# Kernel tuning notes

Hardware: AMD Instinct MI355X
Metric: run time of the kernel (lower is better)

Reference implementation:

```python
import jax, jax.numpy as jnp
import numpy as np

N_ATOM, N_CHI, N_BOND, N_DIR = 119, 3, 5, 3
NUM_LAYER, EMB, FEAT, NG = 5, 300, 256, 4096
N_NODES, N_EDGES = 100000, 200000


def setup_inputs() -> dict:
    key = jax.random.key(0)
    ks = jax.random.split(key, 16)
    N, E = N_NODES, N_EDGES
    r = lambda k, s, sc: jax.random.normal(k, s, jnp.float32) * sc
    inp = {}
    inp["atom_type"] = jax.random.randint(ks[0], (N,), 0, N_ATOM, dtype=jnp.int32)
    inp["chirality"] = jax.random.randint(ks[1], (N,), 0, N_CHI, dtype=jnp.int32)
    inp["edge_index"] = jax.random.randint(ks[2], (2, E), 0, N, dtype=jnp.int32)
    inp["edge_type"] = jax.random.randint(ks[3], (E,), 0, 4, dtype=jnp.int32)
    inp["edge_dir"] = jax.random.randint(ks[4], (E,), 0, N_DIR, dtype=jnp.int32)
    inp["batch"] = jnp.sort(jax.random.randint(ks[5], (N,), 0, NG, dtype=jnp.int32))
    inp["atom_emb1"] = r(ks[6], (N_ATOM, EMB), 0.02)
    inp["atom_emb2"] = r(ks[7], (N_CHI, EMB), 0.02)
    inp["W"] = r(ks[8], (NUM_LAYER, EMB, EMB), 0.05)
    inp["b"] = jnp.zeros((NUM_LAYER, EMB), jnp.float32)
    inp["ee1"] = r(ks[9], (NUM_LAYER, N_BOND, 1), 0.5)
    inp["ee2"] = r(ks[10], (NUM_LAYER, N_DIR, 1), 0.5)
    inp["bn_gamma"] = jnp.ones((NUM_LAYER, EMB), jnp.float32)
    inp["bn_beta"] = jnp.zeros((NUM_LAYER, EMB), jnp.float32)
    inp["feat_W"] = r(ks[11], (EMB, FEAT), 0.05)
    inp["feat_b"] = jnp.zeros((FEAT,), jnp.float32)
    inp["head_W1"] = r(ks[12], (FEAT, FEAT // 2), 0.08)
    inp["head_b1"] = jnp.zeros((FEAT // 2,), jnp.float32)
    inp["head_W2"] = r(ks[13], (FEAT // 2, 2), 0.1)
    inp["head_b2"] = jnp.zeros((2,), jnp.float32)
    return inp


def reference(atom_type, chirality, edge_index, edge_type, edge_dir, batch,
              atom_emb1, atom_emb2, W, b, ee1, ee2, bn_gamma, bn_beta,
              feat_W, feat_b, head_W1, head_b1, head_W2, head_b2):
    N = atom_type.shape[0]
    # add self loops (edge_attr: bond_type=4, direction=0)
    loops = jnp.arange(N, dtype=edge_index.dtype)
    row = jnp.concatenate([edge_index[0], loops])
    col = jnp.concatenate([edge_index[1], loops])
    et = jnp.concatenate([edge_type, jnp.full((N,), 4, edge_type.dtype)])
    ed = jnp.concatenate([edge_dir, jnp.zeros((N,), edge_dir.dtype)])

    h = atom_emb1[atom_type] + atom_emb2[chirality]  # [N, EMB]
    for l in range(NUM_LAYER):
        hx = h @ W[l]                                  # [N, EMB]
        edge_emb = ee1[l][et] + ee2[l][ed]             # [E+N, 1]
        msg = hx[row] + edge_emb                       # gather + broadcast add
        out = jax.ops.segment_sum(msg, col, num_segments=N) + b[l]
        # BatchNorm1d (training-mode batch stats, eps=1e-5)
        mean = out.mean(axis=0)
        var = out.var(axis=0)
        h = bn_gamma[l] * (out - mean) * jax.lax.rsqrt(var + 1e-5) + bn_beta[l]
        if l < NUM_LAYER - 1:
            h = jax.nn.relu(h)  # drop_ratio=0 -> dropout is identity

    # global mean pool over graphs
    sums = jax.ops.segment_sum(h, batch, num_segments=NG)              # [NG, EMB]
    counts = jax.ops.segment_sum(jnp.ones((N, 1), h.dtype), batch, num_segments=NG)
    hg = sums / jnp.maximum(counts, 1.0)

    hf = hg @ feat_W + feat_b                                          # [NG, FEAT]
    pred = jax.nn.softplus(hf @ head_W1 + head_b1) @ head_W2 + head_b2  # [NG, 2]
    return hf, pred
```

## Files before the change

kernel.cpp:

```cpp
#include <hip/hip_runtime.h>
#include <math.h>

typedef unsigned short u16;
typedef unsigned int u32;
typedef short v8s __attribute__((ext_vector_type(8)));
typedef float v4f __attribute__((ext_vector_type(4)));

#define EMB 300
#define SP 320
#define NGRP 4096
#define FEAT 256
#define MT 128
#define NT 160
#define NCOMB 357
#define NREP 32
#define CSB (NREP * 2 * SP)

__device__ __forceinline__ u16 f2bf(float x) {
    u32 u = __float_as_uint(x);
    u += 0x7FFFu + ((u >> 16) & 1u);
    return (u16)(u >> 16);
}
__device__ __forceinline__ float bf2f(u16 h) {
    return __uint_as_float((u32)h << 16);
}
__device__ __forceinline__ void unpack8(uint4 w, float* o) {
    const u32* p = &w.x;
#pragma unroll
    for (int q = 0; q < 4; q++) {
        o[2 * q]     = __uint_as_float(p[q] << 16);
        o[2 * q + 1] = __uint_as_float(p[q] & 0xFFFF0000u);
    }
}
__device__ __forceinline__ v8s clampA(uint4 w, float4 ta, float4 tb) {
    const u32* p = &w.x;
    float t[8] = {ta.x, ta.y, ta.z, ta.w, tb.x, tb.y, tb.z, tb.w};
    u32 o[4];
#pragma unroll
    for (int q = 0; q < 4; q++) {
        float lo = __uint_as_float(p[q] << 16);
        float hi = __uint_as_float(p[q] & 0xFFFF0000u);
        lo = fmaxf(lo, t[2 * q]);
        hi = fmaxf(hi, t[2 * q + 1]);
        o[q] = (__float_as_uint(lo) >> 16) | (__float_as_uint(hi) & 0xFFFF0000u);
    }
    uint4 r = make_uint4(o[0], o[1], o[2], o[3]);
    return *(v8s*)&r;
}
__device__ __forceinline__ void dma16(const u16* g, u16* l) {
    __builtin_amdgcn_global_load_lds(
        (const __attribute__((address_space(1))) unsigned int*)g,
        (__attribute__((address_space(3))) unsigned int*)l, 16, 0, 0);
}

__global__ void k_prep_n(const int* __restrict__ at, const int* __restrict__ ch,
                         int* __restrict__ c9, int* __restrict__ deg,
                         int* __restrict__ cursor, float* __restrict__ cs0, int N) {
    int n = blockIdx.x * blockDim.x + threadIdx.x;
    if (n < N) {
        c9[n] = at[n] * 3 + ch[n];
        deg[n] = 0;
        cursor[n] = 0;
    }
    if (n < CSB) cs0[n] = 0.f;
}

__global__ void k_count(const int* __restrict__ col, int* __restrict__ deg, int E) {
    int e = blockIdx.x * blockDim.x + threadIdx.x;
    if (e < E) atomicAdd(&deg[col[e]], 1);
}

__global__ __launch_bounds__(256) void k_bsum(const int* __restrict__ deg,
                                              int* __restrict__ bsum, int N) {
    int base = blockIdx.x * 1024 + threadIdx.x * 4;
    int s = 0;
    if (base + 3 < N) {
        int4 v = *(const int4*)(deg + base);
        s = v.x + v.y + v.z + v.w;
    } else {
        for (int j = 0; j < 4; j++) if (base + j < N) s += deg[base + j];
    }
    __shared__ int red[256];
    red[threadIdx.x] = s;
    __syncthreads();
    for (int off = 128; off > 0; off >>= 1) {
        if (threadIdx.x < off) red[threadIdx.x] += red[threadIdx.x + off];
        __syncthreads();
    }
    if (threadIdx.x == 0) bsum[blockIdx.x] = red[0];
}

__global__ __launch_bounds__(128) void k_scanb(const int* __restrict__ bsum,
                                               int* __restrict__ boff, int NB) {
    __shared__ int sh[128];
    int t = threadIdx.x;
    int v = (t < NB) ? bsum[t] : 0;
    sh[t] = v;
    __syncthreads();
    for (int off = 1; off < 128; off <<= 1) {
        int add = (t >= off) ? sh[t - off] : 0;
        __syncthreads();
        sh[t] += add;
        __syncthreads();
    }
    if (t < NB) boff[t] = sh[t] - v;
}

__global__ __launch_bounds__(256) void k_indptr(const int* __restrict__ deg,
                                                const int* __restrict__ boff,
                                                int* __restrict__ indptr, int N) {
    int b = blockIdx.x, t = threadIdx.x;
    int base = b * 1024 + t * 4;
    int v[4] = {0, 0, 0, 0};
    if (base + 3 < N) {
        int4 w = *(const int4*)(deg + base);
        v[0] = w.x; v[1] = w.y; v[2] = w.z; v[3] = w.w;
    } else {
        for (int j = 0; j < 4; j++) if (base + j < N) v[j] = deg[base + j];
    }
    int tsum = v[0] + v[1] + v[2] + v[3];
    __shared__ int sh[256];
    sh[t] = tsum;
    __syncthreads();
    for (int off = 1; off < 256; off <<= 1) {
        int add = (t >= off) ? sh[t - off] : 0;
        __syncthreads();
        sh[t] += add;
        __syncthreads();
    }
    int run = boff[b] + sh[t] - tsum;
    for (int j = 0; j < 4; j++) {
        run += v[j];
        if (base + j < N) indptr[base + j + 1] = run;
    }
    if (b == 0 && t == 0) indptr[0] = 0;
}

__global__ void k_fill(const int* __restrict__ row, const int* __restrict__ col,
                       const int* __restrict__ et, const int* __restrict__ ed,
                       const int* __restrict__ indptr, int* __restrict__ cursor,
                       int* __restrict__ packed, int E) {
    int e = blockIdx.x * blockDim.x + threadIdx.x;
    if (e >= E) return;
    int c = col[e];
    int pos = indptr[c] + atomicAdd(&cursor[c], 1);
    packed[pos] = row[e] | ((et[e] * 3 + ed[e]) << 17);
}

__global__ void k_comb(const float* __restrict__ e1, const float* __restrict__ e2,
                       u16* __restrict__ comb) {
    int idx = blockIdx.x * blockDim.x + threadIdx.x;
    if (idx >= NCOMB * 40) return;
    int row = idx / 40, f = idx % 40;
    int at = row / 3, ch = row % 3;
    u32 o[4];
#pragma unroll
    for (int q = 0; q < 4; q++) {
        int c0 = f * 8 + q * 2;
        float x0 = 0.f, x1 = 0.f;
        if (c0 < EMB)     x0 = e1[(size_t)at * EMB + c0] + e2[(size_t)ch * EMB + c0];
        if (c0 + 1 < EMB) x1 = e1[(size_t)at * EMB + c0 + 1] + e2[(size_t)ch * EMB + c0 + 1];
        o[q] = (u32)f2bf(x0) | ((u32)f2bf(x1) << 16);
    }
    *(uint4*)(comb + (size_t)row * SP + f * 8) = make_uint4(o[0], o[1], o[2], o[3]);
}

__global__ __launch_bounds__(320) void k_wprep(
    const float* __restrict__ Wl, const float* __restrict__ cs,
    const float* __restrict__ gamma, const float* __restrict__ beta,
    int ident, int N, u16* __restrict__ Wt, float* __restrict__ srow,
    float* __restrict__ thr) {
    __shared__ float wred[5];
    int n = blockIdx.x;
    int k = threadIdx.x;
    float scv, shv, thv;
    if (ident) {
        scv = (k < EMB) ? 1.f : 0.f;
        shv = 0.f;
        thv = -__builtin_inff();
    } else if (k < EMB) {
        float s1 = 0.f, s2 = 0.f;
        for (int r = 0; r < NREP; r++) {
            s1 += cs[r * 2 * SP + k];
            s2 += cs[r * 2 * SP + SP + k];
        }
        float inv = 1.f / (float)N;
        float mean = s1 * inv;
        float var = s2 * inv - mean * mean;
        float rstd = rsqrtf(fmaxf(var, 0.f) + 1e-5f);
        scv = gamma[k] * rstd;
        shv = beta[k] - mean * scv;
        thv = bf2f(f2bf(-shv / scv));
    } else {
        scv = 0.f; shv = 0.f; thv = -__builtin_inff();
    }
    if (n == 0) thr[k] = thv;

    float w = 0.f;
    if (n < EMB && k < EMB) w = Wl[(size_t)k * EMB + n];
    Wt[(size_t)n * SP + k] = f2bf(w * scv);
    float s = (k < EMB) ? shv * w : 0.f;
#pragma unroll
    for (int o2 = 32; o2 > 0; o2 >>= 1) s += __shfl_down(s, o2);
    if ((k & 63) == 0) wred[k >> 6] = s;
    __syncthreads();
    if (k == 0) {
        float t = wred[0] + wred[1] + wred[2] + wred[3] + wred[4];
        srow[n] = (n < EMB) ? t : 0.f;
    }
}

__global__ void k_finalize(const float* __restrict__ cs,
                           const float* __restrict__ gamma, const float* __restrict__ beta,
                           float* __restrict__ sc, float* __restrict__ sh, int N) {
    int c = threadIdx.x;
    if (c >= SP) return;
    float s1 = 0.f, s2 = 0.f;
    for (int r = 0; r < NREP; r++) {
        s1 += cs[r * 2 * SP + c];
        s2 += cs[r * 2 * SP + SP + c];
    }
    if (c < EMB) {
        float inv = 1.f / (float)N;
        float mean = s1 * inv;
        float var = s2 * inv - mean * mean;
        float rstd = rsqrtf(fmaxf(var, 0.f) + 1e-5f);
        float s = gamma[c] * rstd;
        sc[c] = s;
        sh[c] = beta[c] - mean * s;
    } else {
        sc[c] = 0.f; sh[c] = 0.f;
    }
}

__global__ __launch_bounds__(256) void k_gemm(
    const u16* __restrict__ A, const u16* __restrict__ Wt,
    const float* __restrict__ thr, const float* __restrict__ srow,
    u16* __restrict__ C, int M, const int* __restrict__ rowmap,
    float* __restrict__ zbank) {
    __shared__ __align__(16) u16 sm[18432];

    int m0 = blockIdx.y * MT;
    int n0 = blockIdx.x * NT;
    int tid = threadIdx.x;
    int wave = tid >> 6, lane = tid & 63;
    int wm = wave >> 1, wn = wave & 1;
    int lm = lane & 15, quad = lane >> 4;

    if (blockIdx.x == 0 && blockIdx.y == 0)
        for (int i = tid; i < CSB; i += 256) zbank[i] = 0.f;

    int ar0 = min(m0 + (tid >> 2), M - 1);
    int ar1 = min(m0 + 64 + (tid >> 2), M - 1);
    if (rowmap) { ar0 = rowmap[ar0]; ar1 = rowmap[ar1]; }
    const u16* ag0 = A + (size_t)ar0 * SP + (tid & 3) * 8;
    const u16* ag1 = A + (size_t)ar1 * SP + (tid & 3) * 8;
    const u16* bg0 = Wt + (size_t)(n0 + (tid >> 2)) * SP + (tid & 3) * 8;
    const u16* bg1 = Wt + (size_t)(n0 + 64 + (tid >> 2)) * SP + (tid & 3) * 8;
    const u16* bg2 = Wt + (size_t)(n0 + 128 + (tid >> 2)) * SP + (tid & 3) * 8;

    const float* tp = thr + quad * 8;

    v4f acc[4][5];
#pragma unroll
    for (int nf = 0; nf < 5; nf++) {
        float sv = srow[n0 + wn * 80 + nf * 16 + lm];
#pragma unroll
        for (int mf = 0; mf < 4; mf++)
            acc[mf][nf] = (v4f){sv, sv, sv, sv};
    }

    auto issue = [&](int d, int kt) {
        int ko = kt * 32;
        u16* ad = sm + d * 4096;
        u16* bd = sm + 8192 + d * 5120;
        dma16(ag0 + ko, ad + tid * 8);
        dma16(ag1 + ko, ad + (256 + tid) * 8);
        dma16(bg0 + ko, bd + tid * 8);
        dma16(bg1 + ko, bd + (256 + tid) * 8);
        if (tid < 128) dma16(bg2 + ko, bd + (512 + tid) * 8);
    };

    issue(0, 0);
    for (int kt = 0; kt < SP / 32; kt++) {
        __syncthreads();
        if (kt + 1 < SP / 32) issue((kt + 1) & 1, kt + 1);
        const u16* as = sm + (kt & 1) * 4096;
        const u16* bs = sm + 8192 + (kt & 1) * 5120;
        float4 ta = *(const float4*)(tp + kt * 32);
        float4 tb = *(const float4*)(tp + kt * 32 + 4);
        v8s b[5], a[4];
#pragma unroll
        for (int nf = 0; nf < 5; nf++)
            b[nf] = *(const v8s*)(bs + (wn * 80 + nf * 16 + lm) * 32 + quad * 8);
#pragma unroll
        for (int mf = 0; mf < 4; mf++) {
            uint4 w = *(const uint4*)(as + (wm * 64 + mf * 16 + lm) * 32 + quad * 8);
            a[mf] = clampA(w, ta, tb);
        }
#pragma unroll
        for (int nf = 0; nf < 5; nf++)
#pragma unroll
            for (int mf = 0; mf < 4; mf++)
                acc[mf][nf] = __builtin_amdgcn_mfma_f32_16x16x32_bf16(a[mf], b[nf], acc[mf][nf], 0, 0, 0);
    }

    __syncthreads();
#pragma unroll
    for (int p = 0; p < 2; p++) {
#pragma unroll
        for (int mf2 = 0; mf2 < 2; mf2++) {
            int mf = p * 2 + mf2;
#pragma unroll
            for (int nf = 0; nf < 5; nf++)
#pragma unroll
                for (int r = 0; r < 4; r++)
                    sm[(wm * 32 + mf2 * 16 + quad * 4 + r) * 168 + wn * 80 + nf * 16 + lm] =
                        f2bf(acc[mf][nf][r]);
        }
        __syncthreads();
#pragma unroll
        for (int i = 0; i < 5; i++) {
            int slot = tid + i * 256;
            int lr = slot / 20, cg = slot % 20;
            int grow = m0 + (lr >> 5) * 64 + p * 32 + (lr & 31);
            if (grow < M)
                *(uint4*)(C + (size_t)grow * SP + n0 + cg * 8) =
                    *(const uint4*)(sm + lr * 168 + cg * 8);
        }
        __syncthreads();
    }
}

__global__ __launch_bounds__(320) void k_aggf(
    const u16* __restrict__ Q, const int* __restrict__ indptr,
    const int* __restrict__ packed, const float* __restrict__ e1,
    const float* __restrict__ e2, u16* __restrict__ P,
    float* __restrict__ colstats, int N) {
    __shared__ float tab[15];
    __shared__ float part[8][328];
    int tid = threadIdx.x;
    if (tid < 15) tab[tid] = e1[tid / 3] + e2[tid % 3];
    __syncthreads();
    int f = tid % 40;
    int slot = tid / 40;
    int n = blockIdx.x * 8 + slot;

    float psum[8] = {0, 0, 0, 0, 0, 0, 0, 0};
    float psq[8]  = {0, 0, 0, 0, 0, 0, 0, 0};

    if (n < N) {
        float acc[8];
        unpack8(*(const uint4*)(Q + (size_t)n * SP + f * 8), acc);
        float s = tab[12];
        int i = indptr[n], e = indptr[n + 1];
        int pk = (i < e) ? packed[i] : 0;
        while (i < e) {
            uint4 g = *(const uint4*)(Q + (size_t)(pk & 0x1FFFF) * SP + f * 8);
            int nx = i + 1;
            int pkn = (nx < e) ? packed[nx] : 0;
            float t[8];
            unpack8(g, t);
#pragma unroll
            for (int q = 0; q < 8; q++) acc[q] += t[q];
            s += tab[pk >> 17];
            i = nx; pk = pkn;
        }
        u32 o[4];
#pragma unroll
        for (int q = 0; q < 4; q++) {
            float r0 = acc[2 * q] + s;
            float r1 = acc[2 * q + 1] + s;
            psum[2 * q] = r0;      psum[2 * q + 1] = r1;
            psq[2 * q]  = r0 * r0; psq[2 * q + 1]  = r1 * r1;
            o[q] = (u32)f2bf(r0) | ((u32)f2bf(r1) << 16);
        }
        *(uint4*)(P + (size_t)n * SP + f * 8) = make_uint4(o[0], o[1], o[2], o[3]);
    }

    int rep = (blockIdx.x & (NREP - 1)) * 2 * SP;
#pragma unroll
    for (int j = 0; j < 8; j++) part[slot][f * 8 + j] = psum[j];
    __syncthreads();
    {
        float s = 0.f;
#pragma unroll
        for (int k = 0; k < 8; k++) s += part[k][tid];
        atomicAdd(&colstats[rep + tid], s);
    }
    __syncthreads();
#pragma unroll
    for (int j = 0; j < 8; j++) part[slot][f * 8 + j] = psq[j];
    __syncthreads();
    {
        float s = 0.f;
#pragma unroll
        for (int k = 0; k < 8; k++) s += part[k][tid];
        atomicAdd(&colstats[rep + SP + tid], s);
    }
}

__global__ void k_bounds(const int* __restrict__ batch, int* __restrict__ gstart, int N) {
    int n = blockIdx.x * blockDim.x + threadIdx.x;
    if (n > N) return;
    int bcur = (n < N) ? batch[n] : NGRP;
    int bprev = (n > 0) ? batch[n - 1] : -1;
    for (int g = bprev + 1; g <= bcur; g++) gstart[g] = n;
}

__global__ __launch_bounds__(320) void k_pool(
    const u16* __restrict__ P, const float* __restrict__ sc,
    const float* __restrict__ sh, const int* __restrict__ gstart,
    float* __restrict__ hg) {
    int tid = threadIdx.x;
    int g = blockIdx.x * 8 + tid / 40;
    int f = tid % 40;
    int r0 = gstart[g], r1 = gstart[g + 1];
    int cnt = r1 - r0;
    float acc[8] = {0, 0, 0, 0, 0, 0, 0, 0};
    for (int r = r0; r < r1; r++) {
        float t[8];
        unpack8(*(const uint4*)(P + (size_t)r * SP + f * 8), t);
#pragma unroll
        for (int j = 0; j < 8; j++) acc[j] += t[j];
    }
    float inv = 1.f / (float)max(cnt, 1);
#pragma unroll
    for (int j = 0; j < 8; j++) {
        int c = f * 8 + j;
        if (c < EMB)
            hg[(size_t)g * EMB + c] = (acc[j] * sc[c] + (float)cnt * sh[c]) * inv;
    }
}

__global__ __launch_bounds__(256) void k_feat(const float* __restrict__ hg,
                                              const float* __restrict__ fW,
                                              const float* __restrict__ fb,
                                              float* __restrict__ hf) {
    __shared__ float hgs[16 * EMB];
    int g0 = blockIdx.x * 16;
    int tid = threadIdx.x;
    for (int i = tid; i < 16 * EMB; i += 256) {
        int gi = i / EMB, c = i % EMB;
        hgs[i] = hg[(size_t)(g0 + gi) * EMB + c];
    }
    __syncthreads();
    float acc[16];
    float fbv = fb[tid];
#pragma unroll
    for (int gi = 0; gi < 16; gi++) acc[gi] = fbv;
    for (int k = 0; k < EMB; k++) {
        float w = fW[(size_t)k * FEAT + tid];
#pragma unroll
        for (int gi = 0; gi < 16; gi++) acc[gi] += hgs[gi * EMB + k] * w;
    }
#pragma unroll
    for (int gi = 0; gi < 16; gi++) hf[(size_t)(g0 + gi) * FEAT + tid] = acc[gi];
}

__global__ __launch_bounds__(128) void k_head(const float* __restrict__ hf,
                                              const float* __restrict__ W1,
                                              const float* __restrict__ b1,
                                              const float* __restrict__ W2,
                                              const float* __restrict__ b2,
                                              float* __restrict__ pred) {
    __shared__ float hfs[8 * FEAT];
    __shared__ float sred[2][8][2];
    int g0 = blockIdx.x * 8;
    int tid = threadIdx.x;
    for (int i = tid; i < 8 * FEAT; i += 128) {
        int gi = i >> 8, k = i & 255;
        hfs[i] = hf[(size_t)(g0 + gi) * FEAT + k];
    }
    __syncthreads();
    float acc[8];
    float b1v = b1[tid];
#pragma unroll
    for (int gi = 0; gi < 8; gi++) acc[gi] = b1v;
    for (int k = 0; k < FEAT; k++) {
        float w = W1[(size_t)k * 128 + tid];
#pragma unroll
        for (int gi = 0; gi < 8; gi++) acc[gi] += hfs[gi * FEAT + k] * w;
    }
    float w20 = W2[tid * 2], w21 = W2[tid * 2 + 1];
    int wv = tid >> 6;
#pragma unroll
    for (int gi = 0; gi < 8; gi++) {
        float x = acc[gi];
        float t = fmaxf(x, 0.f) + log1pf(expf(-fabsf(x)));
        float p0 = t * w20, p1 = t * w21;
#pragma unroll
        for (int off = 32; off > 0; off >>= 1) {
            p0 += __shfl_down(p0, off);
            p1 += __shfl_down(p1, off);
        }
        if ((tid & 63) == 0) { sred[wv][gi][0] = p0; sred[wv][gi][1] = p1; }
    }
    __syncthreads();
    if (tid < 16) {
        int gi = tid >> 1, o = tid & 1;
        pred[(size_t)(g0 + gi) * 2 + o] = sred[0][gi][o] + sred[1][gi][o] + b2[o];
    }
}

extern "C" void kernel_launch(void* const* d_in, const int* in_sizes, int n_in,
                              void* d_out, int out_size, void* d_ws, size_t ws_size,
                              hipStream_t stream) {
    const int* atom_type = (const int*)d_in[0];
    const int* chir      = (const int*)d_in[1];
    const int* eidx      = (const int*)d_in[2];
    const int* etype     = (const int*)d_in[3];
    const int* edir      = (const int*)d_in[4];
    const int* batch     = (const int*)d_in[5];
    const float* emb1    = (const float*)d_in[6];
    const float* emb2    = (const float*)d_in[7];
    const float* W       = (const float*)d_in[8];
    const float* ee1     = (const float*)d_in[10];
    const float* ee2     = (const float*)d_in[11];
    const float* gamma   = (const float*)d_in[12];
    const float* beta    = (const float*)d_in[13];
    const float* featW   = (const float*)d_in[14];
    const float* featb   = (const float*)d_in[15];
    const float* hW1     = (const float*)d_in[16];
    const float* hb1     = (const float*)d_in[17];
    const float* hW2     = (const float*)d_in[18];
    const float* hb2     = (const float*)d_in[19];

    int N = in_sizes[0];
    int E = in_sizes[2] / 2;
    const int* erow = eidx;
    const int* ecol = eidx + E;

    size_t off = 0;
    char* base = (char*)d_ws;
    auto carve = [&](size_t bytes) -> void* {
        void* p = base + off;
        off += (bytes + 255) & ~(size_t)255;
        return p;
    };
    u16*   P        = (u16*)  carve((size_t)N * SP * 2);
    u16*   Q        = (u16*)  carve((size_t)N * SP * 2);
    u16*   Wt       = (u16*)  carve((size_t)SP * SP * 2);
    u16*   comb     = (u16*)  carve((size_t)NCOMB * SP * 2);
    int*   c9map    = (int*)  carve((size_t)N * 4);
    int*   deg      = (int*)  carve((size_t)N * 4);
    int*   cursor   = (int*)  carve((size_t)N * 4);
    int*   indptr   = (int*)  carve((size_t)(N + 1) * 4);
    int*   packed   = (int*)  carve((size_t)E * 4);
    int*   bsum     = (int*)  carve(1024 * 4);
    int*   boff     = (int*)  carve(1024 * 4);
    float* cs0      = (float*)carve((size_t)CSB * 4);
    float* cs1      = (float*)carve((size_t)CSB * 4);
    float* scale_bn = (float*)carve(SP * 4);
    float* shift_bn = (float*)carve(SP * 4);
    float* thr_bn   = (float*)carve(SP * 4);
    float* srow     = (float*)carve(SP * 4);
    int*   gstart   = (int*)  carve((size_t)(NGRP + 1) * 4);
    float* hg       = (float*)carve((size_t)NGRP * EMB * 4);

    float* hf   = (float*)d_out;
    float* pred = (float*)d_out + (size_t)NGRP * FEAT;

    int eb = (E + 255) / 256;
    int NB = (N + 1023) / 1024;
    k_prep_n<<<(N + 255) / 256, 256, 0, stream>>>(atom_type, chir, c9map, deg, cursor,
                                                  cs0, N);
    k_count<<<eb, 256, 0, stream>>>(ecol, deg, E);
    k_bsum<<<NB, 256, 0, stream>>>(deg, bsum, N);
    k_scanb<<<1, 128, 0, stream>>>(bsum, boff, NB);
    k_indptr<<<NB, 256, 0, stream>>>(deg, boff, indptr, N);
    k_fill<<<eb, 256, 0, stream>>>(erow, ecol, etype, edir, indptr, cursor, packed, E);

    k_comb<<<(NCOMB * 40 + 255) / 256, 256, 0, stream>>>(emb1, emb2, comb);

    dim3 ggrid(2, (N + MT - 1) / MT);
    int ab = (N + 7) / 8;
    float* banks[2] = {cs0, cs1};
    for (int l = 0; l < 5; l++) {
        float* wb = banks[l & 1];
        float* rb = banks[(l + 1) & 1];
        k_wprep<<<SP, 320, 0, stream>>>(W + (size_t)l * EMB * EMB, rb,
                                        gamma + l * EMB - EMB, beta + l * EMB - EMB,
                                        l == 0 ? 1 : 0, N, Wt, srow, thr_bn);
        if (l == 0)
            k_gemm<<<ggrid, 256, 0, stream>>>(comb, Wt, thr_bn, srow, Q, N, c9map, wb);
        else
            k_gemm<<<ggrid, 256, 0, stream>>>(P, Wt, thr_bn, srow, Q, N, nullptr, wb);
        k_aggf<<<ab, 320, 0, stream>>>(Q, indptr, packed, ee1 + l * 5, ee2 + l * 3, P,
                                       wb, N);
    }

    k_finalize<<<1, SP, 0, stream>>>(banks[4 & 1], gamma + 4 * EMB, beta + 4 * EMB,
                                     scale_bn, shift_bn, N);
    k_bounds<<<(N + 1 + 255) / 256, 256, 0, stream>>>(batch, gstart, N);
    k_pool<<<NGRP / 8, 320, 0, stream>>>(P, scale_bn, shift_bn, gstart, hg);
    k_feat<<<NGRP / 16, 256, 0, stream>>>(hg, featW, featb, hf);
    k_head<<<NGRP / 8, 128, 0, stream>>>(hf, hW1, hb1, hW2, hb2, pred);
}
```

Before: 705.8 us.

## Restructure GEMM to 512 threads with triple-buffered async loads and LDS thresholds

```diff
diff --git a/kernel.cpp b/kernel.cpp
--- a/kernel.cpp
+++ b/kernel.cpp
@@ -233,12 +233,13 @@
     }
 }
 
-__global__ __launch_bounds__(256) void k_gemm(
+__global__ __launch_bounds__(512, 4) void k_gemm(
     const u16* __restrict__ A, const u16* __restrict__ Wt,
     const float* __restrict__ thr, const float* __restrict__ srow,
     u16* __restrict__ C, int M, const int* __restrict__ rowmap,
     float* __restrict__ zbank) {
-    __shared__ __align__(16) u16 sm[18432];
+    __shared__ __align__(16) u16 sm[27648];
+    __shared__ float thrs[SP];
 
     int m0 = blockIdx.y * MT;
     int n0 = blockIdx.x * NT;
@@ -248,87 +249,87 @@
     int lm = lane & 15, quad = lane >> 4;
 
     if (blockIdx.x == 0 && blockIdx.y == 0)
-        for (int i = tid; i < CSB; i += 256) zbank[i] = 0.f;
-
-    int ar0 = min(m0 + (tid >> 2), M - 1);
-    int ar1 = min(m0 + 64 + (tid >> 2), M - 1);
-    if (rowmap) { ar0 = rowmap[ar0]; ar1 = rowmap[ar1]; }
-    const u16* ag0 = A + (size_t)ar0 * SP + (tid & 3) * 8;
-    const u16* ag1 = A + (size_t)ar1 * SP + (tid & 3) * 8;
+        for (int i = tid; i < CSB; i += 512) zbank[i] = 0.f;
+
+    if (tid < SP) thrs[tid] = thr[tid];
+
+    int ar = min(m0 + (tid >> 2), M - 1);
+    if (rowmap) ar = rowmap[ar];
+    const u16* ag  = A  + (size_t)ar * SP + (tid & 3) * 8;
     const u16* bg0 = Wt + (size_t)(n0 + (tid >> 2)) * SP + (tid & 3) * 8;
-    const u16* bg1 = Wt + (size_t)(n0 + 64 + (tid >> 2)) * SP + (tid & 3) * 8;
-    const u16* bg2 = Wt + (size_t)(n0 + 128 + (tid >> 2)) * SP + (tid & 3) * 8;
-
-    const float* tp = thr + quad * 8;
-
-    v4f acc[4][5];
+    const u16* bg1 = Wt + (size_t)(n0 + 128 + (tid >> 2)) * SP + (tid & 3) * 8;
+
+    v4f acc[2][5];
 #pragma unroll
     for (int nf = 0; nf < 5; nf++) {
         float sv = srow[n0 + wn * 80 + nf * 16 + lm];
-#pragma unroll
-        for (int mf = 0; mf < 4; mf++)
-            acc[mf][nf] = (v4f){sv, sv, sv, sv};
-    }
-
-    auto issue = [&](int d, int kt) {
+        acc[0][nf] = (v4f){sv, sv, sv, sv};
+        acc[1][nf] = (v4f){sv, sv, sv, sv};
+    }
+
+    __syncthreads();
+
+    auto issue = [&](int buf, int kt) {
         int ko = kt * 32;
-        u16* ad = sm + d * 4096;
-        u16* bd = sm + 8192 + d * 5120;
-        dma16(ag0 + ko, ad + tid * 8);
-        dma16(ag1 + ko, ad + (256 + tid) * 8);
+        u16* ad = sm + buf * 9216;
+        u16* bd = ad + 4096;
+        dma16(ag + ko, ad + tid * 8);
         dma16(bg0 + ko, bd + tid * 8);
-        dma16(bg1 + ko, bd + (256 + tid) * 8);
-        if (tid < 128) dma16(bg2 + ko, bd + (512 + tid) * 8);
+        if (tid < 128) dma16(bg1 + ko, bd + (512 + tid) * 8);
     };
 
     issue(0, 0);
+    issue(1, 1);
+
     for (int kt = 0; kt < SP / 32; kt++) {
-        __syncthreads();
-        if (kt + 1 < SP / 32) issue((kt + 1) & 1, kt + 1);
-        const u16* as = sm + (kt & 1) * 4096;
-        const u16* bs = sm + 8192 + (kt & 1) * 5120;
-        float4 ta = *(const float4*)(tp + kt * 32);
-        float4 tb = *(const float4*)(tp + kt * 32 + 4);
-        v8s b[5], a[4];
+        if (kt == SP / 32 - 1) {
+            asm volatile("s_waitcnt vmcnt(0)" ::: "memory");
+        } else if (wave < 2) {
+            asm volatile("s_waitcnt vmcnt(3)" ::: "memory");
+        } else {
+            asm volatile("s_waitcnt vmcnt(2)" ::: "memory");
+        }
+        asm volatile("s_barrier" ::: "memory");
+        if (kt + 2 < SP / 32) issue((kt + 2) % 3, kt + 2);
+
+        const u16* as = sm + (kt % 3) * 9216;
+        const u16* bs = as + 4096;
+        float4 ta = *(const float4*)(thrs + kt * 32 + quad * 8);
+        float4 tb = *(const float4*)(thrs + kt * 32 + quad * 8 + 4);
+        v8s b[5], a[2];
 #pragma unroll
         for (int nf = 0; nf < 5; nf++)
             b[nf] = *(const v8s*)(bs + (wn * 80 + nf * 16 + lm) * 32 + quad * 8);
 #pragma unroll
-        for (int mf = 0; mf < 4; mf++) {
-            uint4 w = *(const uint4*)(as + (wm * 64 + mf * 16 + lm) * 32 + quad * 8);
+        for (int mf = 0; mf < 2; mf++) {
+            uint4 w = *(const uint4*)(as + (wm * 32 + mf * 16 + lm) * 32 + quad * 8);
             a[mf] = clampA(w, ta, tb);
         }
 #pragma unroll
         for (int nf = 0; nf < 5; nf++)
 #pragma unroll
-            for (int mf = 0; mf < 4; mf++)
+            for (int mf = 0; mf < 2; mf++)
                 acc[mf][nf] = __builtin_amdgcn_mfma_f32_16x16x32_bf16(a[mf], b[nf], acc[mf][nf], 0, 0, 0);
     }
 
     __syncthreads();
 #pragma unroll
-    for (int p = 0; p < 2; p++) {
-#pragma unroll
-        for (int mf2 = 0; mf2 < 2; mf2++) {
-            int mf = p * 2 + mf2;
-#pragma unroll
-            for (int nf = 0; nf < 5; nf++)
-#pragma unroll
-                for (int r = 0; r < 4; r++)
-                    sm[(wm * 32 + mf2 * 16 + quad * 4 + r) * 168 + wn * 80 + nf * 16 + lm] =
-                        f2bf(acc[mf][nf][r]);
-        }
-        __syncthreads();
-#pragma unroll
-        for (int i = 0; i < 5; i++) {
-            int slot = tid + i * 256;
-            int lr = slot / 20, cg = slot % 20;
-            int grow = m0 + (lr >> 5) * 64 + p * 32 + (lr & 31);
-            if (grow < M)
-                *(uint4*)(C + (size_t)grow * SP + n0 + cg * 8) =
-                    *(const uint4*)(sm + lr * 168 + cg * 8);
-        }
-        __syncthreads();
+    for (int mf = 0; mf < 2; mf++)
+#pragma unroll
+        for (int nf = 0; nf < 5; nf++)
+#pragma unroll
+            for (int r = 0; r < 4; r++)
+                sm[(wm * 32 + mf * 16 + quad * 4 + r) * 168 + wn * 80 + nf * 16 + lm] =
+                    f2bf(acc[mf][nf][r]);
+    __syncthreads();
+#pragma unroll
+    for (int i = 0; i < 5; i++) {
+        int slot = tid + i * 512;
+        int lr = slot / 20, cg = slot % 20;
+        int grow = m0 + lr;
+        if (grow < M)
+            *(uint4*)(C + (size_t)grow * SP + n0 + cg * 8) =
+                *(const uint4*)(sm + lr * 168 + cg * 8);
     }
 }
 
@@ -583,9 +584,9 @@
                                         gamma + l * EMB - EMB, beta + l * EMB - EMB,
                                         l == 0 ? 1 : 0, N, Wt, srow, thr_bn);
         if (l == 0)
-            k_gemm<<<ggrid, 256, 0, stream>>>(comb, Wt, thr_bn, srow, Q, N, c9map, wb);
+            k_gemm<<<ggrid, 512, 0, stream>>>(comb, Wt, thr_bn, srow, Q, N, c9map, wb);
         else
-            k_gemm<<<ggrid, 256, 0, stream>>>(P, Wt, thr_bn, srow, Q, N, nullptr, wb);
+            k_gemm<<<ggrid, 512, 0, stream>>>(P, Wt, thr_bn, srow, Q, N, nullptr, wb);
         k_aggf<<<ab, 320, 0, stream>>>(Q, indptr, packed, ee1 + l * 5, ee2 + l * 3, P,
                                        wb, N);
     }
```

New measurement: 729.6 us. +3.4%, slower.
